# Performance work log

Measured on AMD Instinct MI355X. Metric: run time of the kernel, lower is better.

The kernel has to match this reference:

```python
import jax, jax.numpy as jnp
import numpy as np

ALPHA = 0.2  # LeakyReLU negative slope
NEG_INF = -9e15


def setup_inputs() -> dict:
    key = jax.random.key(0)
    ks = jax.random.split(key, 6)
    B, N, F_IN, F_OUT = 4, 1024, 64, 64
    h = jax.random.normal(ks[0], (B, N, F_IN), dtype=jnp.float32)
    adj = jax.random.randint(ks[1], (B, N, N), 0, 2, dtype=jnp.int32)
    lin_w = jax.random.normal(ks[2], (F_OUT, F_IN), dtype=jnp.float32) * (1.0 / np.sqrt(F_IN))
    lin_b = jax.random.normal(ks[3], (F_OUT,), dtype=jnp.float32) * 0.02
    W_w = jax.random.normal(ks[4], (F_OUT, 2 * F_OUT), dtype=jnp.float32) * (1.0 / np.sqrt(2 * F_OUT))
    a = jax.random.normal(ks[5], (F_OUT, 1), dtype=jnp.float32) * (1.414 / np.sqrt(F_OUT))
    return {"h": h, "adj": adj, "lin_w": lin_w, "lin_b": lin_b, "W_w": W_w, "a": a}


def reference(h, adj, lin_w, lin_b, W_w, a):
    F_OUT = lin_w.shape[0]
    # h' = Linear(h): (B, N, F_OUT)
    hp = jnp.einsum('bni,oi->bno', h, lin_w) + lin_b
    # W @ concat(h_i, h_j) == h_i @ W1^T + h_j @ W2^T  (same math, no 2F concat)
    W1, W2 = W_w[:, :F_OUT], W_w[:, F_OUT:]
    u = jnp.einsum('bnf,of->bno', hp, W1)  # source/row term   (B, N, F_OUT)
    v = jnp.einsum('bnf,of->bno', hp, W2)  # target/col term   (B, N, F_OUT)
    s = u[:, :, None, :] + v[:, None, :, :]        # (B, N, N, F_OUT)
    s = jnp.where(s > 0, s, ALPHA * s)             # LeakyReLU
    e = jnp.einsum('bijf,f->bij', s, a[:, 0])      # (B, N, N)
    e = jnp.where(adj > 0, e, NEG_INF)
    attention = jax.nn.softmax(e, axis=2)
    h_prime = jnp.einsum('bij,bjf->bif', attention, hp)
    return jax.nn.elu(h_prime)
```

## Files before the change

### kernel.cpp

```cpp
#include <hip/hip_runtime.h>
#include <hip/hip_bf16.h>
#include <math.h>

constexpr int B = 4;
constexpr int N = 1024;
constexpr float NEGINF = -9000000000000000.0f;

__global__ __launch_bounds__(512) void gat_prep(
    const float* __restrict__ h, const float* __restrict__ lin_w,
    const float* __restrict__ lin_b, const float* __restrict__ W_w,
    const float* __restrict__ a_g,
    float* __restrict__ hp_g, float* __restrict__ u_out, float* __restrict__ vT_g,
    float* __restrict__ au_out, float* __restrict__ av_out) {
  __shared__ float wlT[64 * 65];
  __shared__ float w1T[64 * 65];
  __shared__ float w2T[64 * 65];
  __shared__ float hs[512];
  __shared__ float hp_s[512];
  __shared__ float v_s[64 * 9];
  __shared__ float a_s[64];

  const int b = blockIdx.x >> 7;
  const int n0 = (blockIdx.x & 127) << 3;
  const int tid = threadIdx.x;
  const int lane = tid & 63, w = tid >> 6;
  const int tn = w, tf = lane;

  if (tid < 64) a_s[tid] = a_g[tid];
  for (int idx = tid; idx < 4096; idx += 512) {
    const int o = idx >> 6, k = idx & 63;
    wlT[k * 65 + o] = lin_w[idx];
    w1T[k * 65 + o] = W_w[o * 128 + k];
    w2T[k * 65 + o] = W_w[o * 128 + 64 + k];
  }
  hs[tid] = h[(((b << 10) + n0) << 6) + tid];
  __syncthreads();

  float hpv = lin_b[tf];
#pragma unroll 8
  for (int k = 0; k < 64; ++k)
    hpv = fmaf(hs[tn * 64 + k], wlT[k * 65 + tf], hpv);
  const int row = (b << 10) + n0 + tn;
  hp_g[(row << 6) + tf] = hpv;
  hp_s[tn * 64 + tf] = hpv;
  __syncthreads();

  float uu = 0.f, vv = 0.f;
#pragma unroll 8
  for (int k = 0; k < 64; ++k) {
    const float hh = hp_s[tn * 64 + k];
    uu = fmaf(hh, w1T[k * 65 + tf], uu);
    vv = fmaf(hh, w2T[k * 65 + tf], vv);
  }
  u_out[(row << 6) + tf] = uu;
  v_s[tf * 9 + tn] = vv;
  float aup = a_s[tf] * uu, avp = a_s[tf] * vv;
#pragma unroll
  for (int off = 32; off; off >>= 1) {
    aup += __shfl_xor(aup, off);
    avp += __shfl_xor(avp, off);
  }
  if (tf == 0) {
    au_out[row] = aup;
    av_out[row] = avp;
  }
  __syncthreads();
  {
    const int f = tid >> 3, n = tid & 7;
    vT_g[(((b << 6) + f) << 10) + n0 + n] = v_s[f * 9 + n];
  }
}

__global__ __launch_bounds__(256) void gat_attn(
    const float* __restrict__ u_g, const float* __restrict__ vT,
    const float* __restrict__ hp, const int* __restrict__ adj,
    const float* __restrict__ a_g, const float* __restrict__ au_g,
    const float* __restrict__ av_g, float* __restrict__ out) {
  __shared__ float p_s[4 * 1024];
  __shared__ float u_s[64 * 4];
  __shared__ float a_s[64];
  __shared__ float au_s[4];
  __shared__ float wred[4][4];
  __shared__ float wsum[4][4];
  __shared__ float rinv_s[4];

  const int b = blockIdx.x >> 8;
  const int i0 = (blockIdx.x & 255) << 2;
  const int tid = threadIdx.x;
  const int lane = tid & 63, w = tid >> 6;
  const int j0 = tid << 2;

  if (tid < 64) a_s[tid] = a_g[tid];
  if (tid < 4) au_s[tid] = au_g[(b << 10) + i0 + tid];
  {
    const int i = tid >> 6, f = tid & 63;
    u_s[f * 4 + i] = u_g[((b << 10) + i0 + i) * 64 + f];
  }
  __syncthreads();

  float e[4][4];
#pragma unroll
  for (int i = 0; i < 4; ++i)
#pragma unroll
    for (int k = 0; k < 4; ++k) e[i][k] = 0.f;

  const float* vb = vT + ((b << 6) << 10) + j0;
#pragma unroll 4
  for (int f = 0; f < 64; ++f) {
    const float af = a_s[f];
    const float4 v4 = *(const float4*)&vb[f << 10];
    const float4 u4 = *(const float4*)&u_s[f * 4];
    const float uu[4] = {u4.x, u4.y, u4.z, u4.w};
    const float vv[4] = {v4.x, v4.y, v4.z, v4.w};
#pragma unroll
    for (int i = 0; i < 4; ++i)
#pragma unroll
      for (int k = 0; k < 4; ++k)
        e[i][k] = fmaf(af, fabsf(uu[i] + vv[k]), e[i][k]);
  }
  const float4 av4 = *(const float4*)&av_g[(b << 10) + j0];
  const float avv[4] = {0.6f * av4.x, 0.6f * av4.y, 0.6f * av4.z, 0.6f * av4.w};
  float au6[4];
#pragma unroll
  for (int i = 0; i < 4; ++i) au6[i] = 0.6f * au_s[i];
  const int* adjb = adj + (((b << 10) + i0) << 10) + j0;
#pragma unroll
  for (int i = 0; i < 4; ++i) {
    const int4 ad = *(const int4*)&adjb[i << 10];
    const int adv[4] = {ad.x, ad.y, ad.z, ad.w};
#pragma unroll
    for (int k = 0; k < 4; ++k) {
      const float ev = fmaf(0.4f, e[i][k], au6[i] + avv[k]);
      e[i][k] = adv[k] > 0 ? ev : NEGINF;
    }
  }

#pragma unroll
  for (int i = 0; i < 4; ++i) {
    float mm = fmaxf(fmaxf(e[i][0], e[i][1]), fmaxf(e[i][2], e[i][3]));
#pragma unroll
    for (int off = 32; off; off >>= 1) mm = fmaxf(mm, __shfl_xor(mm, off));
    if (lane == 0) wred[w][i] = mm;
  }
  __syncthreads();
#pragma unroll
  for (int i = 0; i < 4; ++i) {
    const float mi = fmaxf(fmaxf(wred[0][i], wred[1][i]),
                           fmaxf(wred[2][i], wred[3][i]));
#pragma unroll
    for (int k = 0; k < 4; ++k) e[i][k] = __expf(e[i][k] - mi);
    float ss = e[i][0] + e[i][1] + e[i][2] + e[i][3];
#pragma unroll
    for (int off = 32; off; off >>= 1) ss += __shfl_xor(ss, off);
    if (lane == 0) wsum[w][i] = ss;
  }
  __syncthreads();
  if (tid < 4)
    rinv_s[tid] = 1.0f / (wsum[0][tid] + wsum[1][tid] + wsum[2][tid] + wsum[3][tid]);

#pragma unroll
  for (int k = 0; k < 4; ++k)
    *(float4*)&p_s[(tid << 2) + (k << 10)] =
        make_float4(e[0][k], e[1][k], e[2][k], e[3][k]);
  __syncthreads();

  const int fq = tid & 15, g = tid >> 4;
  float4 acc[4];
#pragma unroll
  for (int i = 0; i < 4; ++i) acc[i] = make_float4(0.f, 0.f, 0.f, 0.f);
  const float* hpb = hp + (b << 16) + (fq << 2);
#pragma unroll 4
  for (int jj = 0; jj < 64; ++jj) {
    const int j = (g << 6) + jj;
    const float4 h4 = *(const float4*)&hpb[j << 6];
    const float4 p4 = *(const float4*)&p_s[(j & ~3) + ((j & 3) << 10)];
    acc[0].x = fmaf(p4.x, h4.x, acc[0].x);
    acc[0].y = fmaf(p4.x, h4.y, acc[0].y);
    acc[0].z = fmaf(p4.x, h4.z, acc[0].z);
    acc[0].w = fmaf(p4.x, h4.w, acc[0].w);
    acc[1].x = fmaf(p4.y, h4.x, acc[1].x);
    acc[1].y = fmaf(p4.y, h4.y, acc[1].y);
    acc[1].z = fmaf(p4.y, h4.z, acc[1].z);
    acc[1].w = fmaf(p4.y, h4.w, acc[1].w);
    acc[2].x = fmaf(p4.z, h4.x, acc[2].x);
    acc[2].y = fmaf(p4.z, h4.y, acc[2].y);
    acc[2].z = fmaf(p4.z, h4.z, acc[2].z);
    acc[2].w = fmaf(p4.z, h4.w, acc[2].w);
    acc[3].x = fmaf(p4.w, h4.x, acc[3].x);
    acc[3].y = fmaf(p4.w, h4.y, acc[3].y);
    acc[3].z = fmaf(p4.w, h4.z, acc[3].z);
    acc[3].w = fmaf(p4.w, h4.w, acc[3].w);
  }
  __syncthreads();
#pragma unroll
  for (int i = 0; i < 4; ++i)
    *(float4*)&p_s[(g << 8) + (i << 6) + (fq << 2)] = acc[i];
  __syncthreads();
  {
    const int i = tid >> 6, f = tid & 63;
    float r = 0.f;
#pragma unroll
    for (int gg = 0; gg < 16; ++gg) r += p_s[(gg << 8) + (i << 6) + f];
    r *= rinv_s[i];
    out[((b << 10) + i0 + i) * 64 + f] = r > 0.f ? r : expm1f(r);
  }
}

extern "C" void kernel_launch(void* const* d_in, const int* in_sizes, int n_in,
                              void* d_out, int out_size, void* d_ws, size_t ws_size,
                              hipStream_t stream) {
  const float* h = (const float*)d_in[0];
  const int* adj = (const int*)d_in[1];
  const float* lin_w = (const float*)d_in[2];
  const float* lin_b = (const float*)d_in[3];
  const float* W_w = (const float*)d_in[4];
  const float* a = (const float*)d_in[5];
  float* outp = (float*)d_out;

  float* ws = (float*)d_ws;
  float* hp = ws;
  float* u = ws + 262144;
  float* vT = ws + 524288;
  float* au = ws + 786432;
  float* av = ws + 790528;

  gat_prep<<<dim3(512), dim3(512), 0, stream>>>(h, lin_w, lin_b, W_w, a,
                                                hp, u, vT, au, av);
  gat_attn<<<dim3(1024), dim3(256), 0, stream>>>(u, vT, hp, adj, a, au, av, outp);
}
```

Measured before the change: 110.3 us.

## Double attention block threads to 512 and reduce partial sums with wave shuffles

The attention kernel now runs 512 threads per block, each handling 2 columns instead of 4, which halves per-thread register use and doubles wave-level parallelism. The P·H accumulation is rearranged to interleave j across 32 groups, with partials reduced in-wave via xor shuffles before a smaller shared-memory cross-wave sum. The trade-off is more threads doing redundant u loads from LDS per column, plus more shuffle work and larger block-level reductions.

```diff
diff --git a/kernel.cpp b/kernel.cpp
--- a/kernel.cpp
+++ b/kernel.cpp
@@ -71,73 +71,70 @@
   }
 }
 
-__global__ __launch_bounds__(256) void gat_attn(
+__global__ __launch_bounds__(512) void gat_attn(
     const float* __restrict__ u_g, const float* __restrict__ vT,
     const float* __restrict__ hp, const int* __restrict__ adj,
     const float* __restrict__ a_g, const float* __restrict__ au_g,
     const float* __restrict__ av_g, float* __restrict__ out) {
   __shared__ float p_s[4 * 1024];
+  __shared__ float wp_s[8 * 256];
   __shared__ float u_s[64 * 4];
   __shared__ float a_s[64];
   __shared__ float au_s[4];
-  __shared__ float wred[4][4];
-  __shared__ float wsum[4][4];
+  __shared__ float wred[8][4];
+  __shared__ float wsum[8][4];
   __shared__ float rinv_s[4];
 
   const int b = blockIdx.x >> 8;
   const int i0 = (blockIdx.x & 255) << 2;
   const int tid = threadIdx.x;
   const int lane = tid & 63, w = tid >> 6;
-  const int j0 = tid << 2;
+  const int j0 = tid << 1;
 
   if (tid < 64) a_s[tid] = a_g[tid];
   if (tid < 4) au_s[tid] = au_g[(b << 10) + i0 + tid];
-  {
+  if (tid < 256) {
     const int i = tid >> 6, f = tid & 63;
     u_s[f * 4 + i] = u_g[((b << 10) + i0 + i) * 64 + f];
   }
   __syncthreads();
 
-  float e[4][4];
-#pragma unroll
-  for (int i = 0; i < 4; ++i)
-#pragma unroll
-    for (int k = 0; k < 4; ++k) e[i][k] = 0.f;
+  float e[4][2];
+#pragma unroll
+  for (int i = 0; i < 4; ++i) { e[i][0] = 0.f; e[i][1] = 0.f; }
 
   const float* vb = vT + ((b << 6) << 10) + j0;
 #pragma unroll 4
   for (int f = 0; f < 64; ++f) {
     const float af = a_s[f];
-    const float4 v4 = *(const float4*)&vb[f << 10];
+    const float2 v2 = *(const float2*)&vb[f << 10];
     const float4 u4 = *(const float4*)&u_s[f * 4];
     const float uu[4] = {u4.x, u4.y, u4.z, u4.w};
-    const float vv[4] = {v4.x, v4.y, v4.z, v4.w};
-#pragma unroll
-    for (int i = 0; i < 4; ++i)
-#pragma unroll
-      for (int k = 0; k < 4; ++k)
-        e[i][k] = fmaf(af, fabsf(uu[i] + vv[k]), e[i][k]);
-  }
-  const float4 av4 = *(const float4*)&av_g[(b << 10) + j0];
-  const float avv[4] = {0.6f * av4.x, 0.6f * av4.y, 0.6f * av4.z, 0.6f * av4.w};
+    const float vv[2] = {v2.x, v2.y};
+#pragma unroll
+    for (int i = 0; i < 4; ++i) {
+      e[i][0] = fmaf(af, fabsf(uu[i] + vv[0]), e[i][0]);
+      e[i][1] = fmaf(af, fabsf(uu[i] + vv[1]), e[i][1]);
+    }
+  }
+  const float2 av2 = *(const float2*)&av_g[(b << 10) + j0];
+  const float avv[2] = {0.6f * av2.x, 0.6f * av2.y};
   float au6[4];
 #pragma unroll
   for (int i = 0; i < 4; ++i) au6[i] = 0.6f * au_s[i];
   const int* adjb = adj + (((b << 10) + i0) << 10) + j0;
 #pragma unroll
   for (int i = 0; i < 4; ++i) {
-    const int4 ad = *(const int4*)&adjb[i << 10];
-    const int adv[4] = {ad.x, ad.y, ad.z, ad.w};
-#pragma unroll
-    for (int k = 0; k < 4; ++k) {
-      const float ev = fmaf(0.4f, e[i][k], au6[i] + avv[k]);
-      e[i][k] = adv[k] > 0 ? ev : NEGINF;
-    }
-  }
-
-#pragma unroll
-  for (int i = 0; i < 4; ++i) {
-    float mm = fmaxf(fmaxf(e[i][0], e[i][1]), fmaxf(e[i][2], e[i][3]));
+    const int2 ad = *(const int2*)&adjb[i << 10];
+    const float e0 = fmaf(0.4f, e[i][0], au6[i] + avv[0]);
+    const float e1 = fmaf(0.4f, e[i][1], au6[i] + avv[1]);
+    e[i][0] = ad.x > 0 ? e0 : NEGINF;
+    e[i][1] = ad.y > 0 ? e1 : NEGINF;
+  }
+
+#pragma unroll
+  for (int i = 0; i < 4; ++i) {
+    float mm = fmaxf(e[i][0], e[i][1]);
 #pragma unroll
     for (int off = 32; off; off >>= 1) mm = fmaxf(mm, __shfl_xor(mm, off));
     if (lane == 0) wred[w][i] = mm;
@@ -145,23 +142,26 @@
   __syncthreads();
 #pragma unroll
   for (int i = 0; i < 4; ++i) {
-    const float mi = fmaxf(fmaxf(wred[0][i], wred[1][i]),
-                           fmaxf(wred[2][i], wred[3][i]));
-#pragma unroll
-    for (int k = 0; k < 4; ++k) e[i][k] = __expf(e[i][k] - mi);
-    float ss = e[i][0] + e[i][1] + e[i][2] + e[i][3];
+    float mi = wred[0][i];
+#pragma unroll
+    for (int ww = 1; ww < 8; ++ww) mi = fmaxf(mi, wred[ww][i]);
+    e[i][0] = __expf(e[i][0] - mi);
+    e[i][1] = __expf(e[i][1] - mi);
+    float ss = e[i][0] + e[i][1];
 #pragma unroll
     for (int off = 32; off; off >>= 1) ss += __shfl_xor(ss, off);
     if (lane == 0) wsum[w][i] = ss;
   }
   __syncthreads();
-  if (tid < 4)
-    rinv_s[tid] = 1.0f / (wsum[0][tid] + wsum[1][tid] + wsum[2][tid] + wsum[3][tid]);
-
-#pragma unroll
-  for (int k = 0; k < 4; ++k)
-    *(float4*)&p_s[(tid << 2) + (k << 10)] =
-        make_float4(e[0][k], e[1][k], e[2][k], e[3][k]);
+  if (tid < 4) {
+    float st = 0.f;
+#pragma unroll
+    for (int ww = 0; ww < 8; ++ww) st += wsum[ww][tid];
+    rinv_s[tid] = 1.0f / st;
+  }
+  *(float4*)&p_s[tid << 2] = make_float4(e[0][0], e[1][0], e[2][0], e[3][0]);
+  *(float4*)&p_s[2048 + (tid << 2)] =
+      make_float4(e[0][1], e[1][1], e[2][1], e[3][1]);
   __syncthreads();
 
   const int fq = tid & 15, g = tid >> 4;
@@ -170,10 +170,10 @@
   for (int i = 0; i < 4; ++i) acc[i] = make_float4(0.f, 0.f, 0.f, 0.f);
   const float* hpb = hp + (b << 16) + (fq << 2);
 #pragma unroll 4
-  for (int jj = 0; jj < 64; ++jj) {
-    const int j = (g << 6) + jj;
+  for (int jj = 0; jj < 32; ++jj) {
+    const int j = (jj << 5) + g;
     const float4 h4 = *(const float4*)&hpb[j << 6];
-    const float4 p4 = *(const float4*)&p_s[(j & ~3) + ((j & 3) << 10)];
+    const float4 p4 = *(const float4*)&p_s[((j & 1) << 11) + ((j >> 1) << 2)];
     acc[0].x = fmaf(p4.x, h4.x, acc[0].x);
     acc[0].y = fmaf(p4.x, h4.y, acc[0].y);
     acc[0].z = fmaf(p4.x, h4.z, acc[0].z);
@@ -191,16 +191,27 @@
     acc[3].z = fmaf(p4.w, h4.z, acc[3].z);
     acc[3].w = fmaf(p4.w, h4.w, acc[3].w);
   }
-  __syncthreads();
-#pragma unroll
-  for (int i = 0; i < 4; ++i)
-    *(float4*)&p_s[(g << 8) + (i << 6) + (fq << 2)] = acc[i];
-  __syncthreads();
-  {
+#pragma unroll
+  for (int i = 0; i < 4; ++i) {
+#pragma unroll
+    for (int off = 16; off <= 32; off <<= 1) {
+      acc[i].x += __shfl_xor(acc[i].x, off);
+      acc[i].y += __shfl_xor(acc[i].y, off);
+      acc[i].z += __shfl_xor(acc[i].z, off);
+      acc[i].w += __shfl_xor(acc[i].w, off);
+    }
+  }
+  if (lane < 16) {
+#pragma unroll
+    for (int i = 0; i < 4; ++i)
+      *(float4*)&wp_s[((w << 2) + i) << 6 | (fq << 2)] = acc[i];
+  }
+  __syncthreads();
+  if (tid < 256) {
     const int i = tid >> 6, f = tid & 63;
     float r = 0.f;
 #pragma unroll
-    for (int gg = 0; gg < 16; ++gg) r += p_s[(gg << 8) + (i << 6) + f];
+    for (int ww = 0; ww < 8; ++ww) r += wp_s[((ww << 2) + i) << 6 | f];
     r *= rinv_s[i];
     out[((b << 10) + i0 + i) * 64 + f] = r > 0.f ? r : expm1f(r);
   }
@@ -226,5 +237,5 @@
 
   gat_prep<<<dim3(512), dim3(512), 0, stream>>>(h, lin_w, lin_b, W_w, a,
                                                 hp, u, vT, au, av);
-  gat_attn<<<dim3(1024), dim3(256), 0, stream>>>(u, vT, hp, adj, a, au, av, outp);
+  gat_attn<<<dim3(1024), dim3(512), 0, stream>>>(u, vT, hp, adj, a, au, av, outp);
 }
```

After: 114.0 us. 1.03x slower.
